# Kernel optimization log

Measured on AMD Instinct MI355X. Metric: run time of the kernel, lower is better.

Reference implementation:

```python
import jax, jax.numpy as jnp
import numpy as np

N = 1048576  # batch
NUM_QUAD = 20


def _mono(x_tail, temp, wd, ws1, bs1, wlast, blast):
    """Monotone dimension: quadrature-summed squared 1-4-4-1 MLP.
    x_tail: [N,1]; temp: [N,4] (or scalar 0.0); wd: [1,4]."""
    q = jnp.linspace(0.0, 1.0, NUM_QUAD + 1)[:NUM_QUAD]  # [Q]
    w = q[1] - q[0]  # uniform quadrature weight (0.05)
    base = x_tail * wd  # [N,4] == (x_tail @ wd) since wd is [1,4]
    h0 = jax.nn.relu(q[:, None, None] * base[None] + temp)       # [Q,N,4]
    h1 = jax.nn.relu(jnp.einsum('qnh,hk->qnk', h0, ws1) + bs1)   # [Q,N,4]
    f = jnp.einsum('qnk,ko->qno', h1, wlast) + blast             # [Q,N,1]
    quad = w * jnp.sum(f * f, axis=0)                            # [N,1]
    return quad * x_tail


def _gen(x, ws0, bs0, ws1, bs1, wlast, blast):
    h0 = jax.nn.relu(x @ ws0 + bs0)
    h1 = jax.nn.relu(h0 @ ws1 + bs1)
    return h1 @ wlast + blast  # [N,1]


def setup_inputs() -> dict:
    key = jax.random.key(0)
    ks = jax.random.split(key, 20)
    shapes = dict(
        x=(N, 2),
        m0_wd=(1, 4), m0_ws1=(4, 4), m0_bs1=(4,), m0_wlast=(4, 1), m0_blast=(1,),
        m1_wd=(1, 4), m1_ws0=(1, 4), m1_bs0=(4,), m1_ws1=(4, 4), m1_bs1=(4,),
        m1_wlast=(4, 1), m1_blast=(1,),
        g0_b=(1,),
        g1_ws0=(2, 4), g1_bs0=(4,), g1_ws1=(4, 4), g1_bs1=(4,),
        g1_wlast=(4, 1), g1_blast=(1,),
    )
    return {name: jax.random.normal(k, shp, dtype=jnp.float32)
            for (name, shp), k in zip(shapes.items(), ks)}


def reference(x, m0_wd, m0_ws1, m0_bs1, m0_wlast, m0_blast,
              m1_wd, m1_ws0, m1_bs0, m1_ws1, m1_bs1, m1_wlast, m1_blast,
              g0_b, g1_ws0, g1_bs0, g1_ws1, g1_bs1, g1_wlast, g1_blast):
    x0 = x[:, 0:1]  # head/tail splits per dimension
    x1 = x[:, 1:2]
    # dim 0: no head, temp = 0; general part is a scalar bias
    y0 = _mono(x0, jnp.float32(0.0), m0_wd, m0_ws1, m0_bs1, m0_wlast, m0_blast) + g0_b
    # dim 1: head is x[:, :1]
    temp1 = x0 @ m1_ws0 + m1_bs0  # [N,4]
    y1 = (_mono(x1, temp1, m1_wd, m1_ws1, m1_bs1, m1_wlast, m1_blast)
          + _gen(x, g1_ws0, g1_bs0, g1_ws1, g1_bs1, g1_wlast, g1_blast))
    return jnp.concatenate([y0, y1], axis=1)  # [N,2]
```

## Files before the change

### kernel.cpp

```cpp
#include <hip/hip_runtime.h>

#define NQ 20

typedef float v4f __attribute__((ext_vector_type(4)));

static __device__ __forceinline__ v4f vbc(float s) { return (v4f){s, s, s, s}; }
static __device__ __forceinline__ v4f vfma4(v4f a, v4f b, v4f c) { return __builtin_elementwise_fma(a, b, c); }
static __device__ __forceinline__ v4f vfmab(v4f a, float b, v4f c) { return __builtin_elementwise_fma(a, vbc(b), c); }
static __device__ __forceinline__ v4f vrelu(v4f a) { return __builtin_elementwise_max(a, vbc(0.0f)); }

__global__ __launch_bounds__(256) void monotone_fused_pk(
    const float4* __restrict__ x4,
    const float* __restrict__ p_m0_wd, const float* __restrict__ p_m0_ws1,
    const float* __restrict__ p_m0_bs1, const float* __restrict__ p_m0_wl,
    const float* __restrict__ p_m0_bl,
    const float* __restrict__ p_m1_wd, const float* __restrict__ p_m1_ws0,
    const float* __restrict__ p_m1_bs0, const float* __restrict__ p_m1_ws1,
    const float* __restrict__ p_m1_bs1, const float* __restrict__ p_m1_wl,
    const float* __restrict__ p_m1_bl,
    const float* __restrict__ p_g0_b,
    const float* __restrict__ p_g1_ws0, const float* __restrict__ p_g1_bs0,
    const float* __restrict__ p_g1_ws1, const float* __restrict__ p_g1_bs1,
    const float* __restrict__ p_g1_wl, const float* __restrict__ p_g1_bl,
    float4* __restrict__ out4, int nchunks, int T)
{
    const int t = blockIdx.x * blockDim.x + threadIdx.x;
    if (t >= T) return;

    const float step = 1.0f / (float)NQ;

    float m0_wd[4], m0_ws1[16], m0_bs1[4], m0_wl[4], m0_bl;
    float m1_wd[4], m1_ws0[4], m1_bs0[4], m1_ws1[16], m1_bs1[4], m1_wl[4], m1_bl;
    float g0b;
    float g1_ws0[8], g1_bs0[4], g1_ws1[16], g1_bs1[4], g1_wl[4], g1_bl;

#pragma unroll
    for (int i = 0; i < 4; ++i) {
        m0_wd[i] = p_m0_wd[i];  m0_bs1[i] = p_m0_bs1[i];  m0_wl[i] = p_m0_wl[i];
        m1_wd[i] = p_m1_wd[i];  m1_ws0[i] = p_m1_ws0[i];  m1_bs0[i] = p_m1_bs0[i];
        m1_bs1[i] = p_m1_bs1[i]; m1_wl[i] = p_m1_wl[i];
        g1_bs0[i] = p_g1_bs0[i]; g1_bs1[i] = p_g1_bs1[i]; g1_wl[i] = p_g1_wl[i];
    }
#pragma unroll
    for (int i = 0; i < 16; ++i) { m0_ws1[i] = p_m0_ws1[i]; m1_ws1[i] = p_m1_ws1[i]; g1_ws1[i] = p_g1_ws1[i]; }
#pragma unroll
    for (int i = 0; i < 8; ++i) g1_ws0[i] = p_g1_ws0[i];
    m0_bl = p_m0_bl[0]; m1_bl = p_m1_bl[0]; g0b = p_g0_b[0]; g1_bl = p_g1_bl[0];

    const float4 a = x4[t];
    const bool has2 = (t + T) < nchunks;
    const float4 b = has2 ? x4[t + T] : a;
    v4f x0 = {a.x, a.z, b.x, b.z};
    v4f x1 = {a.y, a.w, b.y, b.w};

    v4f g;
    {
        v4f h0[4];
#pragma unroll
        for (int j = 0; j < 4; ++j)
            h0[j] = vrelu(vfmab(x1, g1_ws0[4 + j], vfmab(x0, g1_ws0[j], vbc(g1_bs0[j]))));
        v4f f = vbc(g1_bl);
#pragma unroll
        for (int k = 0; k < 4; ++k) {
            v4f v = vbc(g1_bs1[k]);
#pragma unroll
            for (int j = 0; j < 4; ++j) v = vfmab(h0[j], g1_ws1[j * 4 + k], v);
            f = vfmab(vrelu(v), g1_wl[k], f);
        }
        g = f;
    }

    v4f v0[4], dv0[4];
    {
        v4f c[4] = {vbc(0.f), vbc(0.f), vbc(0.f), vbc(0.f)};
#pragma unroll
        for (int h = 0; h < 4; ++h) {
            v4f rb = vrelu(x0 * vbc(m0_wd[h]));
#pragma unroll
            for (int k = 0; k < 4; ++k) c[k] = vfmab(rb, m0_ws1[h * 4 + k], c[k]);
        }
#pragma unroll
        for (int k = 0; k < 4; ++k) { v0[k] = vbc(m0_bs1[k]); dv0[k] = c[k] * vbc(step); }
    }

    v4f u[4], du[4];
#pragma unroll
    for (int h = 0; h < 4; ++h) {
        u[h]  = vfmab(x0, m1_ws0[h], vbc(m1_bs0[h]));
        du[h] = x1 * vbc(m1_wd[h] * step);
    }

    v4f acc0 = vbc(0.f), acc1 = vbc(0.f);
#pragma unroll
    for (int qi = 0; qi < NQ; ++qi) {
        v4f f0 = vbc(m0_bl);
#pragma unroll
        for (int k = 0; k < 4; ++k) f0 = vfmab(vrelu(v0[k]), m0_wl[k], f0);
        acc0 = vfma4(f0, f0, acc0);

        v4f h0[4];
#pragma unroll
        for (int h = 0; h < 4; ++h) h0[h] = vrelu(u[h]);
        v4f f1 = vbc(m1_bl);
#pragma unroll
        for (int k = 0; k < 4; ++k) {
            v4f vv = vbc(m1_bs1[k]);
#pragma unroll
            for (int h = 0; h < 4; ++h) vv = vfmab(h0[h], m1_ws1[h * 4 + k], vv);
            f1 = vfmab(vrelu(vv), m1_wl[k], f1);
        }
        acc1 = vfma4(f1, f1, acc1);

        if (qi != NQ - 1) {
#pragma unroll
            for (int k = 0; k < 4; ++k) v0[k] = v0[k] + dv0[k];
#pragma unroll
            for (int h = 0; h < 4; ++h) u[h] = u[h] + du[h];
        }
    }

    v4f y0 = (acc0 * vbc(step)) * x0 + vbc(g0b);
    v4f y1 = vfma4(acc1 * vbc(step), x1, g);

    const float4 oa = {y0.x, y1.x, y0.y, y1.y};
    out4[t] = oa;
    if (has2) {
        const float4 ob = {y0.z, y1.z, y0.w, y1.w};
        out4[t + T] = ob;
    }
}

extern "C" void kernel_launch(void* const* d_in, const int* in_sizes, int n_in,
                              void* d_out, int out_size, void* d_ws, size_t ws_size,
                              hipStream_t stream) {
    const float* x       = (const float*)d_in[0];
    const float* m0_wd   = (const float*)d_in[1];
    const float* m0_ws1  = (const float*)d_in[2];
    const float* m0_bs1  = (const float*)d_in[3];
    const float* m0_wl   = (const float*)d_in[4];
    const float* m0_bl   = (const float*)d_in[5];
    const float* m1_wd   = (const float*)d_in[6];
    const float* m1_ws0  = (const float*)d_in[7];
    const float* m1_bs0  = (const float*)d_in[8];
    const float* m1_ws1  = (const float*)d_in[9];
    const float* m1_bs1  = (const float*)d_in[10];
    const float* m1_wl   = (const float*)d_in[11];
    const float* m1_bl   = (const float*)d_in[12];
    const float* g0_b    = (const float*)d_in[13];
    const float* g1_ws0  = (const float*)d_in[14];
    const float* g1_bs0  = (const float*)d_in[15];
    const float* g1_ws1  = (const float*)d_in[16];
    const float* g1_bs1  = (const float*)d_in[17];
    const float* g1_wl   = (const float*)d_in[18];
    const float* g1_bl   = (const float*)d_in[19];
    float* out = (float*)d_out;

    const int nrows   = in_sizes[0] / 2;
    const int nchunks = nrows / 2;
    const int T       = (nchunks + 1) / 2;
    const int threads = 256;
    const int blocks  = (T + threads - 1) / threads;

    hipLaunchKernelGGL(monotone_fused_pk, dim3(blocks), dim3(threads), 0, stream,
                       (const float4*)x, m0_wd, m0_ws1, m0_bs1, m0_wl, m0_bl,
                       m1_wd, m1_ws0, m1_bs0, m1_ws1, m1_bs1, m1_wl, m1_bl,
                       g0_b, g1_ws0, g1_bs0, g1_ws1, g1_bs1, g1_wl, g1_bl,
                       (float4*)out, nchunks, T);
}
```

Measured before the change: 26.66 us.

## Halve per-thread rows to two and recompute quadrature points directly

Each thread now handles two rows held in a 2-wide packed vector instead of four, which doubles the thread count and removes the second strided load/store. Quadrature inputs are computed as fma(slope, q, offset) at each step instead of being carried by incremental addition. Launch bounds now request 8 blocks per CU. The aim is lower register pressure and higher occupancy to hide latency. The cost is fewer independent operations per thread for ILP and reloading the weights for twice as many threads.

```diff
diff --git a/kernel.cpp b/kernel.cpp
--- a/kernel.cpp
+++ b/kernel.cpp
@@ -2,14 +2,14 @@
 
 #define NQ 20
 
-typedef float v4f __attribute__((ext_vector_type(4)));
+typedef float v2f __attribute__((ext_vector_type(2)));
 
-static __device__ __forceinline__ v4f vbc(float s) { return (v4f){s, s, s, s}; }
-static __device__ __forceinline__ v4f vfma4(v4f a, v4f b, v4f c) { return __builtin_elementwise_fma(a, b, c); }
-static __device__ __forceinline__ v4f vfmab(v4f a, float b, v4f c) { return __builtin_elementwise_fma(a, vbc(b), c); }
-static __device__ __forceinline__ v4f vrelu(v4f a) { return __builtin_elementwise_max(a, vbc(0.0f)); }
+static __device__ __forceinline__ v2f b2(float s) { return (v2f){s, s}; }
+static __device__ __forceinline__ v2f fma2(v2f a, v2f b, v2f c) { return __builtin_elementwise_fma(a, b, c); }
+static __device__ __forceinline__ v2f fmab(v2f a, float b, v2f c) { return __builtin_elementwise_fma(a, b2(b), c); }
+static __device__ __forceinline__ v2f relu2(v2f a) { return __builtin_elementwise_max(a, b2(0.0f)); }
 
-__global__ __launch_bounds__(256) void monotone_fused_pk(
+__global__ __launch_bounds__(256, 8) void monotone_v2pk(
     const float4* __restrict__ x4,
     const float* __restrict__ p_m0_wd, const float* __restrict__ p_m0_ws1,
     const float* __restrict__ p_m0_bs1, const float* __restrict__ p_m0_wl,
@@ -22,7 +22,7 @@
     const float* __restrict__ p_g1_ws0, const float* __restrict__ p_g1_bs0,
     const float* __restrict__ p_g1_ws1, const float* __restrict__ p_g1_bs1,
     const float* __restrict__ p_g1_wl, const float* __restrict__ p_g1_bl,
-    float4* __restrict__ out4, int nchunks, int T)
+    float4* __restrict__ out4, int T)
 {
     const int t = blockIdx.x * blockDim.x + threadIdx.x;
     if (t >= T) return;
@@ -48,86 +48,73 @@
     m0_bl = p_m0_bl[0]; m1_bl = p_m1_bl[0]; g0b = p_g0_b[0]; g1_bl = p_g1_bl[0];
 
     const float4 a = x4[t];
-    const bool has2 = (t + T) < nchunks;
-    const float4 b = has2 ? x4[t + T] : a;
-    v4f x0 = {a.x, a.z, b.x, b.z};
-    v4f x1 = {a.y, a.w, b.y, b.w};
+    v2f x0 = {a.x, a.z};
+    v2f x1 = {a.y, a.w};
 
-    v4f g;
+    v2f g;
     {
-        v4f h0[4];
+        v2f h0[4];
 #pragma unroll
         for (int j = 0; j < 4; ++j)
-            h0[j] = vrelu(vfmab(x1, g1_ws0[4 + j], vfmab(x0, g1_ws0[j], vbc(g1_bs0[j]))));
-        v4f f = vbc(g1_bl);
+            h0[j] = relu2(fmab(x1, g1_ws0[4 + j], fmab(x0, g1_ws0[j], b2(g1_bs0[j]))));
+        v2f f = b2(g1_bl);
 #pragma unroll
         for (int k = 0; k < 4; ++k) {
-            v4f v = vbc(g1_bs1[k]);
+            v2f v = b2(g1_bs1[k]);
 #pragma unroll
-            for (int j = 0; j < 4; ++j) v = vfmab(h0[j], g1_ws1[j * 4 + k], v);
-            f = vfmab(vrelu(v), g1_wl[k], f);
+            for (int j = 0; j < 4; ++j) v = fmab(h0[j], g1_ws1[j * 4 + k], v);
+            f = fmab(relu2(v), g1_wl[k], f);
         }
         g = f;
     }
 
-    v4f v0[4], dv0[4];
-    {
-        v4f c[4] = {vbc(0.f), vbc(0.f), vbc(0.f), vbc(0.f)};
+    v2f c[4] = {b2(0.f), b2(0.f), b2(0.f), b2(0.f)};
 #pragma unroll
-        for (int h = 0; h < 4; ++h) {
-            v4f rb = vrelu(x0 * vbc(m0_wd[h]));
+    for (int h = 0; h < 4; ++h) {
+        v2f rb = relu2(x0 * b2(m0_wd[h]));
 #pragma unroll
-            for (int k = 0; k < 4; ++k) c[k] = vfmab(rb, m0_ws1[h * 4 + k], c[k]);
-        }
-#pragma unroll
-        for (int k = 0; k < 4; ++k) { v0[k] = vbc(m0_bs1[k]); dv0[k] = c[k] * vbc(step); }
+        for (int k = 0; k < 4; ++k) c[k] = fmab(rb, m0_ws1[h * 4 + k], c[k]);
     }
 
-    v4f u[4], du[4];
+    v2f s1[4], tt[4];
 #pragma unroll
     for (int h = 0; h < 4; ++h) {
-        u[h]  = vfmab(x0, m1_ws0[h], vbc(m1_bs0[h]));
-        du[h] = x1 * vbc(m1_wd[h] * step);
+        s1[h] = x1 * b2(m1_wd[h]);
+        tt[h] = fmab(x0, m1_ws0[h], b2(m1_bs0[h]));
     }
 
-    v4f acc0 = vbc(0.f), acc1 = vbc(0.f);
+    v2f acc0 = b2(0.f), acc1 = b2(0.f);
 #pragma unroll
     for (int qi = 0; qi < NQ; ++qi) {
-        v4f f0 = vbc(m0_bl);
-#pragma unroll
-        for (int k = 0; k < 4; ++k) f0 = vfmab(vrelu(v0[k]), m0_wl[k], f0);
-        acc0 = vfma4(f0, f0, acc0);
+        const float q = (float)qi * step;
 
-        v4f h0[4];
-#pragma unroll
-        for (int h = 0; h < 4; ++h) h0[h] = vrelu(u[h]);
-        v4f f1 = vbc(m1_bl);
+        v2f f0 = b2(m0_bl);
 #pragma unroll
         for (int k = 0; k < 4; ++k) {
-            v4f vv = vbc(m1_bs1[k]);
+            v2f v = relu2(fmab(c[k], q, b2(m0_bs1[k])));
+            f0 = fmab(v, m0_wl[k], f0);
+        }
+        acc0 = fma2(f0, f0, acc0);
+
+        v2f h0[4];
 #pragma unroll
-            for (int h = 0; h < 4; ++h) vv = vfmab(h0[h], m1_ws1[h * 4 + k], vv);
-            f1 = vfmab(vrelu(vv), m1_wl[k], f1);
+        for (int h = 0; h < 4; ++h) h0[h] = relu2(fmab(s1[h], q, tt[h]));
+        v2f f1 = b2(m1_bl);
+#pragma unroll
+        for (int k = 0; k < 4; ++k) {
+            v2f vv = b2(m1_bs1[k]);
+#pragma unroll
+            for (int h = 0; h < 4; ++h) vv = fmab(h0[h], m1_ws1[h * 4 + k], vv);
+            f1 = fmab(relu2(vv), m1_wl[k], f1);
         }
-        acc1 = vfma4(f1, f1, acc1);
-
-        if (qi != NQ - 1) {
-#pragma unroll
-            for (int k = 0; k < 4; ++k) v0[k] = v0[k] + dv0[k];
-#pragma unroll
-            for (int h = 0; h < 4; ++h) u[h] = u[h] + du[h];
-        }
+        acc1 = fma2(f1, f1, acc1);
     }
 
-    v4f y0 = (acc0 * vbc(step)) * x0 + vbc(g0b);
-    v4f y1 = vfma4(acc1 * vbc(step), x1, g);
+    v2f y0 = (acc0 * b2(step)) * x0 + b2(g0b);
+    v2f y1 = fma2(acc1 * b2(step), x1, g);
 
-    const float4 oa = {y0.x, y1.x, y0.y, y1.y};
-    out4[t] = oa;
-    if (has2) {
-        const float4 ob = {y0.z, y1.z, y0.w, y1.w};
-        out4[t + T] = ob;
-    }
+    const float4 o = {y0.x, y1.x, y0.y, y1.y};
+    out4[t] = o;
 }
 
 extern "C" void kernel_launch(void* const* d_in, const int* in_sizes, int n_in,
@@ -155,15 +142,14 @@
     const float* g1_bl   = (const float*)d_in[19];
     float* out = (float*)d_out;
 
-    const int nrows   = in_sizes[0] / 2;
-    const int nchunks = nrows / 2;
-    const int T       = (nchunks + 1) / 2;
+    const int nrows = in_sizes[0] / 2;
+    const int T     = nrows / 2;
     const int threads = 256;
     const int blocks  = (T + threads - 1) / threads;
 
-    hipLaunchKernelGGL(monotone_fused_pk, dim3(blocks), dim3(threads), 0, stream,
+    hipLaunchKernelGGL(monotone_v2pk, dim3(blocks), dim3(threads), 0, stream,
                        (const float4*)x, m0_wd, m0_ws1, m0_bs1, m0_wl, m0_bl,
                        m1_wd, m1_ws0, m1_bs0, m1_ws1, m1_bs1, m1_wl, m1_bl,
                        g0_b, g1_ws0, g1_bs0, g1_ws1, g1_bs1, g1_wl, g1_bl,
-                       (float4*)out, nchunks, T);
+                       (float4*)out, T);
 }
```

Result: no change. 27.09 us (+1.6%).
